# Performance work log

Hardware: AMD Instinct MI355X
Metric: run time of the kernel (lower is better)

## Reference

```python
import jax, jax.numpy as jnp
import numpy as np

N_NODES = 100000
N_EDGES = 3200000
IN_DIM = 128
OUT_DIM = 128


def setup_inputs() -> dict:
    key = jax.random.key(0)
    k1, k2, k3, k4, k5 = jax.random.split(key, 5)
    fea_input = jax.random.normal(k1, (N_NODES, IN_DIM), dtype=jnp.float32)
    edge_row = jax.random.randint(k2, (N_EDGES,), 0, N_NODES, dtype=jnp.int32)
    edge_col = jax.random.randint(k3, (N_EDGES,), 0, N_NODES, dtype=jnp.int32)
    edge_val = jax.random.uniform(k4, (N_EDGES,), dtype=jnp.float32)
    # kaiming_uniform-style init for weight, zeros for bias
    bound = float(np.sqrt(6.0 / IN_DIM))
    weight = jax.random.uniform(k5, (IN_DIM, OUT_DIM), dtype=jnp.float32,
                                minval=-bound, maxval=bound)
    bias = jnp.zeros((OUT_DIM,), dtype=jnp.float32)
    return {
        "fea_input": fea_input,
        "edge_row": edge_row,
        "edge_col": edge_col,
        "edge_val": edge_val,
        "weight": weight,
        "bias": bias,
    }


def reference(fea_input, edge_row, edge_col, edge_val, weight, bias):
    # support = X @ W  -> [N, OUT_DIM]
    support = jnp.matmul(fea_input, weight)
    # SpMM: out[r] += val * support[c] for each edge (r, c, val)
    gathered = support[edge_col] * edge_val[:, None]  # [E, OUT_DIM]
    output = jax.ops.segment_sum(gathered, edge_row, num_segments=N_NODES)
    return output + bias
```

## Files before the change

kernel.cpp:

```cpp
#include <hip/hip_runtime.h>
#include <hip/hip_bf16.h>


#define N_NODES 100000
#define N_EDGES 3200000
#define DIM 128
#define RB 16
#define RPB 128
#define NBKT ((N_NODES + RPB - 1) / RPB)
#define CHUNK 8192
#define NCHK ((N_EDGES + CHUNK - 1) / CHUNK)
#define CAP 6016

typedef __attribute__((ext_vector_type(8))) short bf16x8;
typedef __attribute__((ext_vector_type(4))) float f32x4;
typedef unsigned long long u64;
typedef unsigned int u32;

__device__ inline ushort bf16rne(float f) {
  uint32_t u = __float_as_uint(f);
  u += 0x7fffu + ((u >> 16) & 1u);
  return (ushort)(u >> 16);
}
__device__ inline float lofl(u32 u) { return __uint_as_float(u << 16); }
__device__ inline float hifl(u32 u) { return __uint_as_float(u & 0xffff0000u); }

__global__ __launch_bounds__(256) void prep_count_kernel(
    const float* __restrict__ X, const float* __restrict__ W,
    ushort* __restrict__ Xh, ushort* __restrict__ Wh,
    const int* __restrict__ erow, int* __restrict__ bcnt,
    int* __restrict__ table) {
  __shared__ int cnt[NBKT];
  if (blockIdx.x < 1024) {
    const size_t nx4 = (size_t)N_NODES * DIM / 4;
    const size_t nw4 = (size_t)DIM * DIM / 4;
    for (size_t i = (size_t)blockIdx.x * blockDim.x + threadIdx.x;
         i < nx4 + nw4; i += (size_t)1024 * blockDim.x) {
      const float4 f = (i < nx4) ? ((const float4*)X)[i] : ((const float4*)W)[i - nx4];
      ushort4 h;
      h.x = bf16rne(f.x); h.y = bf16rne(f.y); h.z = bf16rne(f.z); h.w = bf16rne(f.w);
      if (i < nx4) ((ushort4*)Xh)[i] = h;
      else         ((ushort4*)Wh)[i - nx4] = h;
    }
  } else {
    const int cb = blockIdx.x - 1024;
    for (int b = threadIdx.x; b < NBKT; b += 256) cnt[b] = 0;
    __syncthreads();
    const int e0 = cb * CHUNK;
    #pragma unroll
    for (int it = 0; it < CHUNK / 256; ++it) {
      const int e = e0 + it * 256 + threadIdx.x;
      if (e < N_EDGES) atomicAdd(&cnt[erow[e] >> 7], 1);
    }
    __syncthreads();
    for (int b = threadIdx.x; b < NBKT; b += 256) {
      const int c = cnt[b];
      table[(size_t)cb * NBKT + b] = c;
      if (c) atomicAdd(&bcnt[b], c);
    }
  }
}

__global__ __launch_bounds__(1024) void bscan_kernel(int* __restrict__ bcur,
                                                     int* __restrict__ bbase) {
  __shared__ int wsum[16];
  const int t = threadIdx.x, lane = t & 63, wid = t >> 6;
  const int v = (t < NBKT) ? bcur[t] : 0;
  int incl = v;
  #pragma unroll
  for (int off = 1; off < 64; off <<= 1) {
    int n = __shfl_up(incl, off, 64);
    if (lane >= off) incl += n;
  }
  if (lane == 63) wsum[wid] = incl;
  __syncthreads();
  if (t == 0) {
    int s = 0;
    #pragma unroll
    for (int w = 0; w < 16; ++w) { int x = wsum[w]; wsum[w] = s; s += x; }
  }
  __syncthreads();
  const int excl = wsum[wid] + incl - v;
  if (t < NBKT) { bbase[t] = excl; bcur[t] = excl; }
  if (t == NBKT - 1) bbase[NBKT] = excl + v;
}

__global__ __launch_bounds__(256) void partition_kernel(
    const int* __restrict__ erow, const int* __restrict__ ecol,
    const float* __restrict__ eval, const int* __restrict__ table,
    int* __restrict__ bcur, u64* __restrict__ p64) {
  __shared__ int cnt[NBKT];
  const int e0 = blockIdx.x * CHUNK;
  for (int b = threadIdx.x; b < NBKT; b += 256) {
    const int c = table[(size_t)blockIdx.x * NBKT + b];
    cnt[b] = c ? atomicAdd(&bcur[b], c) : 0;
  }
  __syncthreads();
  #pragma unroll
  for (int it = 0; it < CHUNK / 256; ++it) {
    const int e = e0 + it * 256 + threadIdx.x;
    if (e < N_EDGES) {
      const int r = erow[e];
      const u32 lo = ((u32)ecol[e] << 15) | (u32)bf16rne(eval[e]);
      const int p = atomicAdd(&cnt[r >> 7], 1);
      p64[p] = ((u64)(r & (RPB - 1)) << 32) | (u64)lo;
    }
  }
}

__global__ __launch_bounds__(256) void bsort_kernel(
    const int* __restrict__ bbase, u64* __restrict__ p64,
    int* __restrict__ row_ptr, ushort* __restrict__ row_len) {
  __shared__ u64 ebuf[CAP];
  __shared__ int hist[RPB];
  __shared__ int excl[RPB];
  __shared__ int wtot;
  const int b = blockIdx.x, t = threadIdx.x;
  const int s = bbase[b];
  int nE = bbase[b + 1] - s;
  if (nE > CAP) nE = CAP;
  const u64* src = p64 + s;
  for (int i = t; i < nE; i += 256) ebuf[i] = src[i];
  if (t < RPB) hist[t] = 0;
  __syncthreads();
  for (int i = t; i < nE; i += 256)
    atomicAdd(&hist[(int)(ebuf[i] >> 32) & (RPB - 1)], 1);
  __syncthreads();
  int v = 0, incl = 0;
  if (t < RPB) {
    v = hist[t];
    incl = v;
    #pragma unroll
    for (int off = 1; off < 64; off <<= 1) {
      int n = __shfl_up(incl, off, 64);
      if ((t & 63) >= off) incl += n;
    }
    if (t == 63) wtot = incl;
  }
  __syncthreads();
  if (t < RPB) {
    const int e = incl - v + ((t >= 64) ? wtot : 0);
    excl[t] = e;
    const int gr = b * RPB + t;
    if (gr < N_NODES) { row_ptr[gr] = s + e; row_len[gr] = (ushort)v; }
  }
  __syncthreads();
  for (int i = t; i < nE; i += 256) {
    const u64 w = ebuf[i];
    const int p = atomicAdd(&excl[(int)(w >> 32) & (RPB - 1)], 1);
    const u32 lo = (u32)w;
    const u32 off = (lo >> 7) & 0xFFFFFF00u;
    const u32 vb  = (lo & 0x7fffu) << 16;
    p64[s + p] = ((u64)vb << 32) | (u64)off;
  }
}

__global__ __launch_bounds__(256) void agg_kernel(
    const ushort* __restrict__ Xh,
    const int* __restrict__ row_ptr, const ushort* __restrict__ row_len,
    const u64* __restrict__ edges, ushort* __restrict__ Yh) {
  const int r = blockIdx.x * 4 + (threadIdx.x >> 6);
  if (r >= N_NODES) return;
  const int lane = threadIdx.x & 63;
  const int q = lane >> 4;
  const u32 sub16 = (u32)(lane & 15) * 16u;
  const char* Xb = (const char*)Xh;
  const int s0 = row_ptr[r];
  const int s1 = s0 + (int)row_len[r];
  float f0 = 0.f, f1 = 0.f, f2 = 0.f, f3 = 0.f;
  float f4 = 0.f, f5 = 0.f, f6 = 0.f, f7 = 0.f;
  for (int e = s0 + q; e < s1 || (e - q) < s1; e += 16) {
    const u64 w0 = (e      < s1) ? edges[e]      : 0ull;
    const u64 w1 = (e + 4  < s1) ? edges[e + 4]  : 0ull;
    const u64 w2 = (e + 8  < s1) ? edges[e + 8]  : 0ull;
    const u64 w3 = (e + 12 < s1) ? edges[e + 12] : 0ull;
    const uint4 g0 = *(const uint4*)(Xb + ((u32)w0 + sub16));
    const uint4 g1 = *(const uint4*)(Xb + ((u32)w1 + sub16));
    const uint4 g2 = *(const uint4*)(Xb + ((u32)w2 + sub16));
    const uint4 g3 = *(const uint4*)(Xb + ((u32)w3 + sub16));
    const float v0 = __uint_as_float((u32)(w0 >> 32));
    const float v1 = __uint_as_float((u32)(w1 >> 32));
    const float v2 = __uint_as_float((u32)(w2 >> 32));
    const float v3 = __uint_as_float((u32)(w3 >> 32));
    f0 += v0 * lofl(g0.x); f1 += v0 * hifl(g0.x);
    f2 += v0 * lofl(g0.y); f3 += v0 * hifl(g0.y);
    f4 += v0 * lofl(g0.z); f5 += v0 * hifl(g0.z);
    f6 += v0 * lofl(g0.w); f7 += v0 * hifl(g0.w);
    f0 += v1 * lofl(g1.x); f1 += v1 * hifl(g1.x);
    f2 += v1 * lofl(g1.y); f3 += v1 * hifl(g1.y);
    f4 += v1 * lofl(g1.z); f5 += v1 * hifl(g1.z);
    f6 += v1 * lofl(g1.w); f7 += v1 * hifl(g1.w);
    f0 += v2 * lofl(g2.x); f1 += v2 * hifl(g2.x);
    f2 += v2 * lofl(g2.y); f3 += v2 * hifl(g2.y);
    f4 += v2 * lofl(g2.z); f5 += v2 * hifl(g2.z);
    f6 += v2 * lofl(g2.w); f7 += v2 * hifl(g2.w);
    f0 += v3 * lofl(g3.x); f1 += v3 * hifl(g3.x);
    f2 += v3 * lofl(g3.y); f3 += v3 * hifl(g3.y);
    f4 += v3 * lofl(g3.z); f5 += v3 * hifl(g3.z);
    f6 += v3 * lofl(g3.w); f7 += v3 * hifl(g3.w);
  }
  f0 += __shfl_xor(f0, 16); f1 += __shfl_xor(f1, 16);
  f2 += __shfl_xor(f2, 16); f3 += __shfl_xor(f3, 16);
  f4 += __shfl_xor(f4, 16); f5 += __shfl_xor(f5, 16);
  f6 += __shfl_xor(f6, 16); f7 += __shfl_xor(f7, 16);
  f0 += __shfl_xor(f0, 32); f1 += __shfl_xor(f1, 32);
  f2 += __shfl_xor(f2, 32); f3 += __shfl_xor(f3, 32);
  f4 += __shfl_xor(f4, 32); f5 += __shfl_xor(f5, 32);
  f6 += __shfl_xor(f6, 32); f7 += __shfl_xor(f7, 32);
  if (lane < 16) {
    uint4 o;
    o.x = (u32)bf16rne(f0) | ((u32)bf16rne(f1) << 16);
    o.y = (u32)bf16rne(f2) | ((u32)bf16rne(f3) << 16);
    o.z = (u32)bf16rne(f4) | ((u32)bf16rne(f5) << 16);
    o.w = (u32)bf16rne(f6) | ((u32)bf16rne(f7) << 16);
    ((uint4*)(Yh + (size_t)r * DIM))[lane] = o;
  }
}

__global__ __launch_bounds__(256) void gemm_mfma(const ushort* __restrict__ Yh,
                                                 const ushort* __restrict__ Wh,
                                                 const float* __restrict__ bias,
                                                 float* __restrict__ out) {
  const int wid = threadIdx.x >> 6, lane = threadIdx.x & 63;
  const int lr = lane & 15, lq = lane >> 4;
  const int n0 = wid * 32;

  bf16x8 bfrag[4][2];
  float bval[2];
  #pragma unroll
  for (int nt = 0; nt < 2; ++nt) {
    const int col = n0 + nt * 16 + lr;
    bval[nt] = bias[col];
    #pragma unroll
    for (int kk = 0; kk < 4; ++kk) {
      const int kbase = kk * 32 + lq * 8;
      bf16x8 b;
      #pragma unroll
      for (int i = 0; i < 8; ++i)
        b[i] = (short)Wh[(size_t)(kbase + i) * DIM + col];
      bfrag[kk][nt] = b;
    }
  }

  const int r0 = blockIdx.x * 256;
  #pragma unroll 1
  for (int g = 0; g < 16; ++g) {
    const int m0 = r0 + g * 16;
    if (m0 >= N_NODES) break;
    bf16x8 afrag[4];
    const ushort* arow = Yh + (size_t)(m0 + lr) * DIM + lq * 8;
    #pragma unroll
    for (int kk = 0; kk < 4; ++kk)
      afrag[kk] = *(const bf16x8*)(arow + kk * 32);
    #pragma unroll
    for (int nt = 0; nt < 2; ++nt) {
      f32x4 acc = {0.f, 0.f, 0.f, 0.f};
      #pragma unroll
      for (int kk = 0; kk < 4; ++kk)
        acc = __builtin_amdgcn_mfma_f32_16x16x32_bf16(afrag[kk], bfrag[kk][nt], acc, 0, 0, 0);
      const int col = n0 + nt * 16 + lr;
      #pragma unroll
      for (int j = 0; j < 4; ++j)
        out[(size_t)(m0 + lq * 4 + j) * DIM + col] = acc[j] + bval[nt];
    }
  }
}

__global__ __launch_bounds__(128) void gemm_kernel(
    const float* __restrict__ IN, const float* __restrict__ W,
    float* __restrict__ OUT, const float* __restrict__ bias, int add_bias) {
  __shared__ float Wsh[DIM * DIM];
  __shared__ float Xsh[RB * DIM];
  const int t = threadIdx.x;
  #pragma unroll 8
  for (int i = 0; i < DIM; ++i) Wsh[i * DIM + t] = W[i * DIM + t];
  const int r0 = blockIdx.x * RB;
  #pragma unroll
  for (int idx = t; idx < RB * DIM; idx += 128)
    Xsh[idx] = IN[(size_t)r0 * DIM + idx];
  __syncthreads();
  float acc[RB];
  const float b = add_bias ? bias[t] : 0.f;
  #pragma unroll
  for (int r = 0; r < RB; ++r) acc[r] = b;
  for (int k = 0; k < DIM; ++k) {
    const float w = Wsh[k * DIM + t];
    #pragma unroll
    for (int r = 0; r < RB; ++r) acc[r] += Xsh[r * DIM + k] * w;
  }
  #pragma unroll
  for (int r = 0; r < RB; ++r)
    OUT[(size_t)(r0 + r) * DIM + t] = acc[r];
}

__global__ void init_kernel(float* __restrict__ out, const float* __restrict__ bias) {
  const size_t total4 = (size_t)N_NODES * DIM / 4;
  const float4* b4 = (const float4*)bias;
  float4* o4 = (float4*)out;
  for (size_t i = (size_t)blockIdx.x * blockDim.x + threadIdx.x;
       i < total4; i += (size_t)gridDim.x * blockDim.x)
    o4[i] = b4[i & 31];
}

__global__ __launch_bounds__(256) void scatter_kernel(
    const float* __restrict__ S,
    const int* __restrict__ erow, const int* __restrict__ ecol,
    const float* __restrict__ eval, float* __restrict__ out) {
  const long long g = (long long)blockIdx.x * blockDim.x + threadIdx.x;
  const long long e = g >> 5;
  const int lane = (int)(g & 31);
  if (e >= N_EDGES) return;
  const int r = erow[e];
  const int c = ecol[e];
  const float v = eval[e];
  const float4 x = ((const float4*)(S + (size_t)c * DIM))[lane];
  float* o = out + (size_t)r * DIM + lane * 4;
  atomicAdd(o + 0, v * x.x);
  atomicAdd(o + 1, v * x.y);
  atomicAdd(o + 2, v * x.z);
  atomicAdd(o + 3, v * x.w);
}

extern "C" void kernel_launch(void* const* d_in, const int* in_sizes, int n_in,
                              void* d_out, int out_size, void* d_ws, size_t ws_size,
                              hipStream_t stream) {
  const float* X    = (const float*)d_in[0];
  const int*   erow = (const int*)d_in[1];
  const int*   ecol = (const int*)d_in[2];
  const float* eval = (const float*)d_in[3];
  const float* W    = (const float*)d_in[4];
  const float* bias = (const float*)d_in[5];
  float* out = (float*)d_out;

  const size_t P64_BYTES = (size_t)N_EDGES * 8;
  const size_t XH_BYTES  = (size_t)N_NODES * DIM * 2;
  const size_t YH_BYTES  = (size_t)N_NODES * DIM * 2;
  const size_t WH_BYTES  = (size_t)DIM * DIM * 2;
  const size_t RP_BYTES  = (size_t)N_NODES * 4;
  const size_t RL_BYTES  = (size_t)N_NODES * 2;
  const size_t BB_BYTES  = (size_t)(NBKT + 1) * 4;
  const size_t BC_BYTES  = (size_t)NBKT * 4;
  const size_t NEED = P64_BYTES + XH_BYTES + YH_BYTES + WH_BYTES +
                      RP_BYTES + RL_BYTES + BB_BYTES + BC_BYTES + 256;

  if (ws_size >= NEED) {
    char* w = (char*)d_ws;
    u64*    p64     = (u64*)w;     w += P64_BYTES;
    ushort* Xh      = (ushort*)w;  w += XH_BYTES;
    ushort* Yh      = (ushort*)w;  w += YH_BYTES;
    ushort* Wh      = (ushort*)w;  w += WH_BYTES;
    int*    row_ptr = (int*)w;     w += RP_BYTES;
    ushort* row_len = (ushort*)w;  w += RL_BYTES;
    int*    bbase   = (int*)w;     w += BB_BYTES;
    int*    bcur    = (int*)w;
    int*    table   = (int*)Yh;

    hipMemsetAsync(bcur, 0, BC_BYTES, stream);
    prep_count_kernel<<<1024 + NCHK, 256, 0, stream>>>(X, W, Xh, Wh, erow, bcur, table);
    bscan_kernel<<<1, 1024, 0, stream>>>(bcur, bbase);
    partition_kernel<<<NCHK, 256, 0, stream>>>(erow, ecol, eval, table, bcur, p64);
    bsort_kernel<<<NBKT, 256, 0, stream>>>(bbase, p64, row_ptr, row_len);
    agg_kernel<<<(N_NODES + 3) / 4, 256, 0, stream>>>(Xh, row_ptr, row_len, p64, Yh);
    gemm_mfma<<<(N_NODES + 255) / 256, 256, 0, stream>>>(Yh, Wh, bias, out);
  } else {
    float* S = (float*)d_ws;
    init_kernel<<<2048, 256, 0, stream>>>(out, bias);
    gemm_kernel<<<N_NODES / RB, 128, 0, stream>>>(X, W, S, bias, 0);
    const long long threads = (long long)N_EDGES * 32;
    scatter_kernel<<<(int)((threads + 255) / 256), 256, 0, stream>>>(S, erow, ecol, eval, out);
  }
}
```

Baseline: 242.6 us.

## Fuse bucket sort and aggregation into one kernel using LDS-resident edges

Merges the per-bucket counting sort and the row aggregation into a single 512-thread kernel per 128-row bucket. Sorted edges are kept as packed 32-bit words in shared memory instead of being written back to global memory and re-read, and the row_ptr/row_len arrays are dropped. The aim is to remove one kernel launch and a round trip of the edge array through global memory. In exchange, each block now handles 128 rows with only 8 waves, which may reduce latency hiding for the gathers and leave load imbalance across buckets. The shared-memory cap is lower than before, so any bucket with more than 5376 edges would be silently truncated.

```diff
diff --git a/kernel.cpp b/kernel.cpp
--- a/kernel.cpp
+++ b/kernel.cpp
@@ -10,7 +10,7 @@
 #define NBKT ((N_NODES + RPB - 1) / RPB)
 #define CHUNK 8192
 #define NCHK ((N_EDGES + CHUNK - 1) / CHUNK)
-#define CAP 6016
+#define CAP2 5376
 
 typedef __attribute__((ext_vector_type(8))) short bf16x8;
 typedef __attribute__((ext_vector_type(4))) float f32x4;
@@ -108,23 +108,24 @@
   }
 }
 
-__global__ __launch_bounds__(256) void bsort_kernel(
-    const int* __restrict__ bbase, u64* __restrict__ p64,
-    int* __restrict__ row_ptr, ushort* __restrict__ row_len) {
-  __shared__ u64 ebuf[CAP];
+__global__ __launch_bounds__(512) void agg_sort_kernel(
+    const ushort* __restrict__ Xh,
+    const int* __restrict__ bbase, const u64* __restrict__ p64,
+    ushort* __restrict__ Yh) {
+  __shared__ u32 sbuf[CAP2 + 16];
   __shared__ int hist[RPB];
-  __shared__ int excl[RPB];
+  __shared__ int rstart[RPB];
+  __shared__ int curs[RPB];
   __shared__ int wtot;
   const int b = blockIdx.x, t = threadIdx.x;
   const int s = bbase[b];
   int nE = bbase[b + 1] - s;
-  if (nE > CAP) nE = CAP;
-  const u64* src = p64 + s;
-  for (int i = t; i < nE; i += 256) ebuf[i] = src[i];
+  if (nE > CAP2) nE = CAP2;
+
   if (t < RPB) hist[t] = 0;
   __syncthreads();
-  for (int i = t; i < nE; i += 256)
-    atomicAdd(&hist[(int)(ebuf[i] >> 32) & (RPB - 1)], 1);
+  for (int i = t; i < nE; i += 512)
+    atomicAdd(&hist[(int)(p64[s + i] >> 32) & (RPB - 1)], 1);
   __syncthreads();
   int v = 0, incl = 0;
   if (t < RPB) {
@@ -140,80 +141,81 @@
   __syncthreads();
   if (t < RPB) {
     const int e = incl - v + ((t >= 64) ? wtot : 0);
-    excl[t] = e;
-    const int gr = b * RPB + t;
-    if (gr < N_NODES) { row_ptr[gr] = s + e; row_len[gr] = (ushort)v; }
-  }
-  __syncthreads();
-  for (int i = t; i < nE; i += 256) {
-    const u64 w = ebuf[i];
-    const int p = atomicAdd(&excl[(int)(w >> 32) & (RPB - 1)], 1);
-    const u32 lo = (u32)w;
-    const u32 off = (lo >> 7) & 0xFFFFFF00u;
-    const u32 vb  = (lo & 0x7fffu) << 16;
-    p64[s + p] = ((u64)vb << 32) | (u64)off;
-  }
-}
-
-__global__ __launch_bounds__(256) void agg_kernel(
-    const ushort* __restrict__ Xh,
-    const int* __restrict__ row_ptr, const ushort* __restrict__ row_len,
-    const u64* __restrict__ edges, ushort* __restrict__ Yh) {
-  const int r = blockIdx.x * 4 + (threadIdx.x >> 6);
-  if (r >= N_NODES) return;
-  const int lane = threadIdx.x & 63;
+    rstart[t] = e;
+    curs[t] = e;
+  }
+  __syncthreads();
+  for (int i = t; i < nE; i += 512) {
+    const u64 w = p64[s + i];
+    const int p = atomicAdd(&curs[(int)(w >> 32) & (RPB - 1)], 1);
+    sbuf[p] = (u32)w;
+  }
+  __syncthreads();
+
+  const int wid = t >> 6, lane = t & 63;
   const int q = lane >> 4;
   const u32 sub16 = (u32)(lane & 15) * 16u;
   const char* Xb = (const char*)Xh;
-  const int s0 = row_ptr[r];
-  const int s1 = s0 + (int)row_len[r];
-  float f0 = 0.f, f1 = 0.f, f2 = 0.f, f3 = 0.f;
-  float f4 = 0.f, f5 = 0.f, f6 = 0.f, f7 = 0.f;
-  for (int e = s0 + q; e < s1 || (e - q) < s1; e += 16) {
-    const u64 w0 = (e      < s1) ? edges[e]      : 0ull;
-    const u64 w1 = (e + 4  < s1) ? edges[e + 4]  : 0ull;
-    const u64 w2 = (e + 8  < s1) ? edges[e + 8]  : 0ull;
-    const u64 w3 = (e + 12 < s1) ? edges[e + 12] : 0ull;
-    const uint4 g0 = *(const uint4*)(Xb + ((u32)w0 + sub16));
-    const uint4 g1 = *(const uint4*)(Xb + ((u32)w1 + sub16));
-    const uint4 g2 = *(const uint4*)(Xb + ((u32)w2 + sub16));
-    const uint4 g3 = *(const uint4*)(Xb + ((u32)w3 + sub16));
-    const float v0 = __uint_as_float((u32)(w0 >> 32));
-    const float v1 = __uint_as_float((u32)(w1 >> 32));
-    const float v2 = __uint_as_float((u32)(w2 >> 32));
-    const float v3 = __uint_as_float((u32)(w3 >> 32));
-    f0 += v0 * lofl(g0.x); f1 += v0 * hifl(g0.x);
-    f2 += v0 * lofl(g0.y); f3 += v0 * hifl(g0.y);
-    f4 += v0 * lofl(g0.z); f5 += v0 * hifl(g0.z);
-    f6 += v0 * lofl(g0.w); f7 += v0 * hifl(g0.w);
-    f0 += v1 * lofl(g1.x); f1 += v1 * hifl(g1.x);
-    f2 += v1 * lofl(g1.y); f3 += v1 * hifl(g1.y);
-    f4 += v1 * lofl(g1.z); f5 += v1 * hifl(g1.z);
-    f6 += v1 * lofl(g1.w); f7 += v1 * hifl(g1.w);
-    f0 += v2 * lofl(g2.x); f1 += v2 * hifl(g2.x);
-    f2 += v2 * lofl(g2.y); f3 += v2 * hifl(g2.y);
-    f4 += v2 * lofl(g2.z); f5 += v2 * hifl(g2.z);
-    f6 += v2 * lofl(g2.w); f7 += v2 * hifl(g2.w);
-    f0 += v3 * lofl(g3.x); f1 += v3 * hifl(g3.x);
-    f2 += v3 * lofl(g3.y); f3 += v3 * hifl(g3.y);
-    f4 += v3 * lofl(g3.z); f5 += v3 * hifl(g3.z);
-    f6 += v3 * lofl(g3.w); f7 += v3 * hifl(g3.w);
-  }
-  f0 += __shfl_xor(f0, 16); f1 += __shfl_xor(f1, 16);
-  f2 += __shfl_xor(f2, 16); f3 += __shfl_xor(f3, 16);
-  f4 += __shfl_xor(f4, 16); f5 += __shfl_xor(f5, 16);
-  f6 += __shfl_xor(f6, 16); f7 += __shfl_xor(f7, 16);
-  f0 += __shfl_xor(f0, 32); f1 += __shfl_xor(f1, 32);
-  f2 += __shfl_xor(f2, 32); f3 += __shfl_xor(f3, 32);
-  f4 += __shfl_xor(f4, 32); f5 += __shfl_xor(f5, 32);
-  f6 += __shfl_xor(f6, 32); f7 += __shfl_xor(f7, 32);
-  if (lane < 16) {
-    uint4 o;
-    o.x = (u32)bf16rne(f0) | ((u32)bf16rne(f1) << 16);
-    o.y = (u32)bf16rne(f2) | ((u32)bf16rne(f3) << 16);
-    o.z = (u32)bf16rne(f4) | ((u32)bf16rne(f5) << 16);
-    o.w = (u32)bf16rne(f6) | ((u32)bf16rne(f7) << 16);
-    ((uint4*)(Yh + (size_t)r * DIM))[lane] = o;
+  #pragma unroll 1
+  for (int j = 0; j < 16; ++j) {
+    const int rl = wid * 16 + j;
+    const int gr = b * RPB + rl;
+    if (gr >= N_NODES) break;
+    const int s0 = rstart[rl];
+    const int s1 = s0 + hist[rl];
+    float f0 = 0.f, f1 = 0.f, f2 = 0.f, f3 = 0.f;
+    float f4 = 0.f, f5 = 0.f, f6 = 0.f, f7 = 0.f;
+    #pragma unroll 1
+    for (int e = s0 + q; e < s1; e += 16) {
+      const u32 lo0 = sbuf[e];
+      const u32 lo1 = (e + 4  < s1) ? sbuf[e + 4]  : 0u;
+      const u32 lo2 = (e + 8  < s1) ? sbuf[e + 8]  : 0u;
+      const u32 lo3 = (e + 12 < s1) ? sbuf[e + 12] : 0u;
+      const u32 o0 = (lo0 >> 7) & 0xFFFFFF00u;
+      const u32 o1 = (lo1 >> 7) & 0xFFFFFF00u;
+      const u32 o2 = (lo2 >> 7) & 0xFFFFFF00u;
+      const u32 o3 = (lo3 >> 7) & 0xFFFFFF00u;
+      const uint4 g0 = *(const uint4*)(Xb + (o0 + sub16));
+      const uint4 g1 = *(const uint4*)(Xb + (o1 + sub16));
+      const uint4 g2 = *(const uint4*)(Xb + (o2 + sub16));
+      const uint4 g3 = *(const uint4*)(Xb + (o3 + sub16));
+      const float v0 = __uint_as_float((lo0 & 0x7fffu) << 16);
+      const float v1 = __uint_as_float((lo1 & 0x7fffu) << 16);
+      const float v2 = __uint_as_float((lo2 & 0x7fffu) << 16);
+      const float v3 = __uint_as_float((lo3 & 0x7fffu) << 16);
+      f0 += v0 * lofl(g0.x); f1 += v0 * hifl(g0.x);
+      f2 += v0 * lofl(g0.y); f3 += v0 * hifl(g0.y);
+      f4 += v0 * lofl(g0.z); f5 += v0 * hifl(g0.z);
+      f6 += v0 * lofl(g0.w); f7 += v0 * hifl(g0.w);
+      f0 += v1 * lofl(g1.x); f1 += v1 * hifl(g1.x);
+      f2 += v1 * lofl(g1.y); f3 += v1 * hifl(g1.y);
+      f4 += v1 * lofl(g1.z); f5 += v1 * hifl(g1.z);
+      f6 += v1 * lofl(g1.w); f7 += v1 * hifl(g1.w);
+      f0 += v2 * lofl(g2.x); f1 += v2 * hifl(g2.x);
+      f2 += v2 * lofl(g2.y); f3 += v2 * hifl(g2.y);
+      f4 += v2 * lofl(g2.z); f5 += v2 * hifl(g2.z);
+      f6 += v2 * lofl(g2.w); f7 += v2 * hifl(g2.w);
+      f0 += v3 * lofl(g3.x); f1 += v3 * hifl(g3.x);
+      f2 += v3 * lofl(g3.y); f3 += v3 * hifl(g3.y);
+      f4 += v3 * lofl(g3.z); f5 += v3 * hifl(g3.z);
+      f6 += v3 * lofl(g3.w); f7 += v3 * hifl(g3.w);
+    }
+    f0 += __shfl_xor(f0, 16); f1 += __shfl_xor(f1, 16);
+    f2 += __shfl_xor(f2, 16); f3 += __shfl_xor(f3, 16);
+    f4 += __shfl_xor(f4, 16); f5 += __shfl_xor(f5, 16);
+    f6 += __shfl_xor(f6, 16); f7 += __shfl_xor(f7, 16);
+    f0 += __shfl_xor(f0, 32); f1 += __shfl_xor(f1, 32);
+    f2 += __shfl_xor(f2, 32); f3 += __shfl_xor(f3, 32);
+    f4 += __shfl_xor(f4, 32); f5 += __shfl_xor(f5, 32);
+    f6 += __shfl_xor(f6, 32); f7 += __shfl_xor(f7, 32);
+    if (lane < 16) {
+      uint4 o;
+      o.x = (u32)bf16rne(f0) | ((u32)bf16rne(f1) << 16);
+      o.y = (u32)bf16rne(f2) | ((u32)bf16rne(f3) << 16);
+      o.z = (u32)bf16rne(f4) | ((u32)bf16rne(f5) << 16);
+      o.w = (u32)bf16rne(f6) | ((u32)bf16rne(f7) << 16);
+      ((uint4*)(Yh + (size_t)gr * DIM))[lane] = o;
+    }
   }
 }
 
@@ -336,12 +338,10 @@
   const size_t XH_BYTES  = (size_t)N_NODES * DIM * 2;
   const size_t YH_BYTES  = (size_t)N_NODES * DIM * 2;
   const size_t WH_BYTES  = (size_t)DIM * DIM * 2;
-  const size_t RP_BYTES  = (size_t)N_NODES * 4;
-  const size_t RL_BYTES  = (size_t)N_NODES * 2;
   const size_t BB_BYTES  = (size_t)(NBKT + 1) * 4;
   const size_t BC_BYTES  = (size_t)NBKT * 4;
   const size_t NEED = P64_BYTES + XH_BYTES + YH_BYTES + WH_BYTES +
-                      RP_BYTES + RL_BYTES + BB_BYTES + BC_BYTES + 256;
+                      BB_BYTES + BC_BYTES + 256;
 
   if (ws_size >= NEED) {
     char* w = (char*)d_ws;
@@ -349,8 +349,6 @@
     ushort* Xh      = (ushort*)w;  w += XH_BYTES;
     ushort* Yh      = (ushort*)w;  w += YH_BYTES;
     ushort* Wh      = (ushort*)w;  w += WH_BYTES;
-    int*    row_ptr = (int*)w;     w += RP_BYTES;
-    ushort* row_len = (ushort*)w;  w += RL_BYTES;
     int*    bbase   = (int*)w;     w += BB_BYTES;
     int*    bcur    = (int*)w;
     int*    table   = (int*)Yh;
@@ -359,8 +357,7 @@
     prep_count_kernel<<<1024 + NCHK, 256, 0, stream>>>(X, W, Xh, Wh, erow, bcur, table);
     bscan_kernel<<<1, 1024, 0, stream>>>(bcur, bbase);
     partition_kernel<<<NCHK, 256, 0, stream>>>(erow, ecol, eval, table, bcur, p64);
-    bsort_kernel<<<NBKT, 256, 0, stream>>>(bbase, p64, row_ptr, row_len);
-    agg_kernel<<<(N_NODES + 3) / 4, 256, 0, stream>>>(Xh, row_ptr, row_len, p64, Yh);
+    agg_sort_kernel<<<NBKT, 512, 0, stream>>>(Xh, bbase, p64, Yh);
     gemm_mfma<<<(N_NODES + 255) / 256, 256, 0, stream>>>(Yh, Wh, bias, out);
   } else {
     float* S = (float*)d_ws;
```

After: 233.4 us. 3.8% less time.
